# Performance work log

Measured on AMD Instinct MI355X. Metric: run time of the kernel, lower is better.

Reference implementation:

```python
import jax, jax.numpy as jnp
import numpy as np

NEG_NUM = -10000.0

def setup_inputs() -> dict:
    key = jax.random.key(0)
    k1, k2, k3, k4, k5, k6 = jax.random.split(key, 6)
    batch, enc_len = 32, 2048
    ctx_size, query_size, att_hid = 1024, 1024, 512
    in_dim = ctx_size + query_size
    ctx = jax.random.normal(k1, (batch, enc_len, ctx_size), dtype=jnp.float32)
    query = jax.random.normal(k2, (batch, query_size), dtype=jnp.float32)
    mask = jax.random.randint(k3, (batch, enc_len), 0, 2, dtype=jnp.int32)
    # Linear params (stored as (in, out) for x @ W + b)
    s1 = 1.0 / np.sqrt(in_dim)
    W1 = jax.random.uniform(k4, (in_dim, att_hid), jnp.float32, -s1, s1)
    b1 = jnp.zeros((att_hid,), jnp.float32)
    s2 = 1.0 / np.sqrt(att_hid)
    W2 = jax.random.uniform(k5, (att_hid, 1), jnp.float32, -s2, s2)
    b2 = jnp.zeros((1,), jnp.float32)
    return {"ctx": ctx, "query": query, "W1": W1, "b1": b1, "W2": W2, "b2": b2, "mask": mask}

def reference(ctx, query, W1, b1, W2, b2, mask):
    # ctx: (B, S, Dc), query: (B, Dq)
    B, S, Dc = ctx.shape
    Dq = query.shape[-1]
    # Equivalent to concat([ctx, query_expanded]) @ W1: split W1 into ctx/query blocks
    Wc, Wq = W1[:Dc], W1[Dc:]
    hidden = jnp.tanh(jnp.einsum('bsd,dh->bsh', ctx, Wc)
                      + (query @ Wq)[:, None, :] + b1)      # (B, S, H)
    score = jnp.einsum('bsh,h->bs', hidden, W2[:, 0]) + b2[0]  # (B, S)
    score = jnp.where(mask == 0, NEG_NUM, score)
    p_ctx = jax.nn.softmax(score, axis=-1)                   # (B, S)
    expected_ctx = jnp.einsum('bs,bsd->bd', p_ctx, ctx)      # (B, Dc)
    return (expected_ctx, p_ctx)
```

## Files before the change

kernel.cpp:

```cpp
#include <hip/hip_runtime.h>

typedef __bf16 bf16;
typedef __attribute__((ext_vector_type(8))) __bf16 bf16x8;
typedef __attribute__((ext_vector_type(4))) __bf16 bf16x4;
typedef __attribute__((ext_vector_type(4))) float f32x4;

#define B_  32
#define S_  2048
#define DC  1024
#define DQ  1024
#define H_  512
#define M_  (B_*S_)

#define BM  64

__global__ __launch_bounds__(256) void k_prep(const float* __restrict__ W1,
                                              const float* __restrict__ query,
                                              const float* __restrict__ b1,
                                              bf16* __restrict__ WcT2,
                                              float* __restrict__ qb) {
    const int bid = blockIdx.x, tid = threadIdx.x;
    if (bid < 256) {
        __shared__ bf16 t[32 * 68];
        const int kb = bid >> 3;
        const int cb = bid & 7;
        #pragma unroll
        for (int i = 0; i < 2; ++i) {
            int idx = i * 256 + tid;
            int k  = idx >> 4;
            int h4 = (idx & 15) * 4;
            const float4 v = *(const float4*)(W1 + ((size_t)(kb * 32 + k)) * H_ + cb * 64 + h4);
            bf16x4 pk = { (bf16)v.x, (bf16)v.y, (bf16)v.z, (bf16)v.w };
            *(bf16x4*)(&t[k * 68 + h4]) = pk;
        }
        __syncthreads();
        const int col = tid >> 2;
        const int kk0 = (tid & 3) * 8;
        bf16x8 o;
        #pragma unroll
        for (int j = 0; j < 8; ++j) o[j] = t[(kk0 + j) * 68 + col];
        *(bf16x8*)(WcT2 + (size_t)kb * 16384 + (size_t)(cb * 64 + col) * 32 + kk0) = o;
    } else {
        const int r = bid - 256;
        const int hblk = r & 7;
        const int b    = r >> 3;
        __shared__ float q[DQ];
        __shared__ float red[256];
        #pragma unroll
        for (int i = 0; i < 4; ++i)
            q[tid + i * 256] = query[(size_t)b * DQ + tid + i * 256];
        __syncthreads();
        const int h  = hblk * 64 + (tid & 63);
        const int kc = tid >> 6;
        const float* w = W1 + (size_t)DC * H_ + (size_t)(kc * 256) * H_ + h;
        const float* qv = q + kc * 256;
        float acc = 0.0f;
        #pragma unroll 8
        for (int k = 0; k < 256; ++k)
            acc = fmaf(qv[k], w[(size_t)k * H_], acc);
        red[tid] = acc;
        __syncthreads();
        if (tid < 64)
            qb[(size_t)b * H_ + hblk * 64 + tid] =
                red[tid] + red[tid + 64] + red[tid + 128] + red[tid + 192] + b1[hblk * 64 + tid];
    }
}

__global__ __launch_bounds__(256, 2) void k_gemm(const float* __restrict__ ctx,
                                                 const bf16*  __restrict__ WcT2,
                                                 const float* __restrict__ qb,
                                                 const float* __restrict__ W2,
                                                 float* __restrict__ score) {
    __shared__ float red[BM * 4];

    const int tid  = threadIdx.x;
    const int mblk = blockIdx.x;
    const size_t row_base = (size_t)mblk * BM;
    const int b = mblk >> 5;

    const int lane = tid & 63;
    const int wn   = tid >> 6;
    const int l16  = lane & 15;
    const int quad = lane >> 4;

    f32x4 acc[4][8] = {};

    const float* arow[4];
    #pragma unroll
    for (int mf = 0; mf < 4; ++mf)
        arow[mf] = ctx + (row_base + mf * 16 + l16) * (size_t)DC + quad * 8;
    const bf16* bptr = WcT2 + (size_t)(wn * 128 + l16) * 32 + quad * 8;

    float4 av0[2][4], av1[2][4];
    #pragma unroll
    for (int mf = 0; mf < 4; ++mf) {
        av0[0][mf] = *(const float4*)(arow[mf]);
        av1[0][mf] = *(const float4*)(arow[mf] + 4);
    }

    #pragma unroll 2
    for (int kb = 0; kb < 32; ++kb) {
        const int cur = kb & 1, nxt = cur ^ 1;
        bf16x8 bF[8];
        #pragma unroll
        for (int nf = 0; nf < 8; ++nf)
            bF[nf] = *(const bf16x8*)(bptr + (size_t)kb * 16384 + nf * 512);
        if (kb < 31) {
            #pragma unroll
            for (int mf = 0; mf < 4; ++mf) {
                av0[nxt][mf] = *(const float4*)(arow[mf] + (kb + 1) * 32);
                av1[nxt][mf] = *(const float4*)(arow[mf] + (kb + 1) * 32 + 4);
            }
        }
        bf16x8 aF[4];
        #pragma unroll
        for (int mf = 0; mf < 4; ++mf) {
            const float4 v0 = av0[cur][mf], v1 = av1[cur][mf];
            aF[mf] = bf16x8{ (bf16)v0.x, (bf16)v0.y, (bf16)v0.z, (bf16)v0.w,
                             (bf16)v1.x, (bf16)v1.y, (bf16)v1.z, (bf16)v1.w };
        }
        #pragma unroll
        for (int mf = 0; mf < 4; ++mf)
            #pragma unroll
            for (int nf = 0; nf < 8; ++nf)
                acc[mf][nf] = __builtin_amdgcn_mfma_f32_16x16x32_bf16(aF[mf], bF[nf], acc[mf][nf], 0, 0, 0);
    }

    float qv[8], wv[8];
    #pragma unroll
    for (int nf = 0; nf < 8; ++nf) {
        int c = wn * 128 + nf * 16 + l16;
        qv[nf] = qb[(size_t)b * H_ + c];
        wv[nf] = W2[c];
    }
    #pragma unroll
    for (int mf = 0; mf < 4; ++mf) {
        #pragma unroll
        for (int r = 0; r < 4; ++r) {
            float s = 0.0f;
            #pragma unroll
            for (int nf = 0; nf < 8; ++nf) {
                float x = acc[mf][nf][r] + qv[nf];
                float t = 1.0f - 2.0f / (1.0f + __expf(2.0f * x));
                s = fmaf(t, wv[nf], s);
            }
            s += __shfl_xor(s, 1);
            s += __shfl_xor(s, 2);
            s += __shfl_xor(s, 4);
            s += __shfl_xor(s, 8);
            if (l16 == 0)
                red[(mf * 16 + quad * 4 + r) * 4 + wn] = s;
        }
    }
    __syncthreads();
    if (tid < BM)
        score[row_base + tid] = red[tid * 4] + red[tid * 4 + 1] + red[tid * 4 + 2] + red[tid * 4 + 3];
}

__global__ __launch_bounds__(256) void k_softmax(const float* __restrict__ score,
                                                 const float* __restrict__ b2,
                                                 const int*   __restrict__ mask,
                                                 float* __restrict__ p_out) {
    int b = blockIdx.x, tid = threadIdx.x;
    __shared__ float red[256];
    float loc[8];
    float b2v = b2[0];
    float mx = -1e30f;
    #pragma unroll
    for (int i = 0; i < 8; ++i) {
        size_t r = (size_t)b * S_ + i * 256 + tid;
        float v = score[r] + b2v;
        if (mask[r] == 0) v = -10000.0f;
        loc[i] = v;
        mx = fmaxf(mx, v);
    }
    red[tid] = mx; __syncthreads();
    for (int o = 128; o > 0; o >>= 1) {
        if (tid < o) red[tid] = fmaxf(red[tid], red[tid + o]);
        __syncthreads();
    }
    mx = red[0]; __syncthreads();
    float se = 0.0f;
    #pragma unroll
    for (int i = 0; i < 8; ++i) {
        float e = __expf(loc[i] - mx);
        loc[i] = e;
        se += e;
    }
    red[tid] = se; __syncthreads();
    for (int o = 128; o > 0; o >>= 1) {
        if (tid < o) red[tid] += red[tid + o];
        __syncthreads();
    }
    float inv = 1.0f / red[0];
    #pragma unroll
    for (int i = 0; i < 8; ++i)
        p_out[(size_t)b * S_ + i * 256 + tid] = loc[i] * inv;
}

__global__ __launch_bounds__(256) void k_expected(const float* __restrict__ ctx,
                                                  const float* __restrict__ p,
                                                  float* __restrict__ partial) {
    const int sb = blockIdx.x, b = blockIdx.y, tid = threadIdx.x;
    __shared__ float ps[64];
    if (tid < 64) ps[tid] = p[(size_t)b * S_ + sb * 64 + tid];
    __syncthreads();
    const float* base = ctx + ((size_t)b * S_ + sb * 64) * DC + tid * 4;
    float ax = 0.f, ay = 0.f, az = 0.f, aw = 0.f;
    #pragma unroll 8
    for (int s = 0; s < 64; ++s) {
        const float4 v = *(const float4*)(base + (size_t)s * DC);
        float w = ps[s];
        ax = fmaf(w, v.x, ax);
        ay = fmaf(w, v.y, ay);
        az = fmaf(w, v.z, az);
        aw = fmaf(w, v.w, aw);
    }
    float4 o = { ax, ay, az, aw };
    *(float4*)(partial + ((size_t)(b * 32 + sb)) * DC + tid * 4) = o;
}

__global__ __launch_bounds__(256) void k_reduce(const float* __restrict__ partial,
                                                float* __restrict__ out) {
    const int cq = blockIdx.x, b = blockIdx.y, tid = threadIdx.x;
    const int c = cq * 256 + tid;
    float acc = 0.f;
    #pragma unroll
    for (int sb = 0; sb < 32; ++sb)
        acc += partial[((size_t)(b * 32 + sb)) * DC + c];
    out[(size_t)b * DC + c] = acc;
}

extern "C" void kernel_launch(void* const* d_in, const int* in_sizes, int n_in,
                              void* d_out, int out_size, void* d_ws, size_t ws_size,
                              hipStream_t stream) {
    (void)in_sizes; (void)n_in; (void)out_size; (void)ws_size;
    const float* ctx   = (const float*)d_in[0];
    const float* query = (const float*)d_in[1];
    const float* W1    = (const float*)d_in[2];
    const float* b1    = (const float*)d_in[3];
    const float* W2    = (const float*)d_in[4];
    const float* b2    = (const float*)d_in[5];
    const int*   mask  = (const int*)d_in[6];

    float* out      = (float*)d_out;
    float* expected = out;
    float* p_out    = out + 32768;

    char* w = (char*)d_ws;
    bf16*  WcT2      = (bf16*)w;
    float* qb        = (float*)(w + (1 << 20));
    float* score     = (float*)(w + (1 << 20) + (64 << 10));
    float* partial_e = (float*)(w + (1 << 20) + (320 << 10));

    k_prep    <<<512, 256, 0, stream>>>(W1, query, b1, WcT2, qb);
    k_gemm    <<<M_ / BM, 256, 0, stream>>>(ctx, WcT2, qb, W2, score);
    k_softmax <<<B_, 256, 0, stream>>>(score, b2, mask, p_out);
    k_expected<<<dim3(32, B_), 256, 0, stream>>>(ctx, p_out, partial_e);
    k_reduce  <<<dim3(4, B_), 256, 0, stream>>>(partial_e, expected);
}
```

Before: 550.6 us.

## Stage ctx tiles in LDS and cache a bf16 ctx copy for the weighted sum

```diff
diff --git a/kernel.cpp b/kernel.cpp
--- a/kernel.cpp
+++ b/kernel.cpp
@@ -13,6 +13,9 @@
 #define M_  (B_*S_)
 
 #define BM  64
+#define BK  32
+
+__device__ __forceinline__ int aoff(int s) { return s * 8 + (s >> 3) * 2; }
 
 __global__ __launch_bounds__(256) void k_prep(const float* __restrict__ W1,
                                               const float* __restrict__ query,
@@ -66,11 +69,14 @@
     }
 }
 
+template<bool STORE>
 __global__ __launch_bounds__(256, 2) void k_gemm(const float* __restrict__ ctx,
                                                  const bf16*  __restrict__ WcT2,
                                                  const float* __restrict__ qb,
                                                  const float* __restrict__ W2,
-                                                 float* __restrict__ score) {
+                                                 float* __restrict__ score,
+                                                 bf16* __restrict__ ctxb) {
+    __shared__ bf16 As[2][2176];
     __shared__ float red[BM * 4];
 
     const int tid  = threadIdx.x;
@@ -85,45 +91,53 @@
 
     f32x4 acc[4][8] = {};
 
-    const float* arow[4];
-    #pragma unroll
-    for (int mf = 0; mf < 4; ++mf)
-        arow[mf] = ctx + (row_base + mf * 16 + l16) * (size_t)DC + quad * 8;
+    const int srow = (tid >> 6) * 16 + (tid & 15);
+    const int sq   = (tid >> 4) & 3;
+    const float* asrc = ctx + (row_base + srow) * (size_t)DC + sq * 8;
+    bf16* adst = STORE ? (ctxb + (row_base + srow) * (size_t)DC + sq * 8) : (bf16*)nullptr;
+    const int awr = aoff(tid);
+    int ard[4];
+    #pragma unroll
+    for (int mf = 0; mf < 4; ++mf) ard[mf] = aoff(mf * 64 + lane);
     const bf16* bptr = WcT2 + (size_t)(wn * 128 + l16) * 32 + quad * 8;
 
-    float4 av0[2][4], av1[2][4];
-    #pragma unroll
-    for (int mf = 0; mf < 4; ++mf) {
-        av0[0][mf] = *(const float4*)(arow[mf]);
-        av1[0][mf] = *(const float4*)(arow[mf] + 4);
-    }
-
-    #pragma unroll 2
+    {
+        const float4 v0 = *(const float4*)(asrc);
+        const float4 v1 = *(const float4*)(asrc + 4);
+        bf16x8 a8 = { (bf16)v0.x, (bf16)v0.y, (bf16)v0.z, (bf16)v0.w,
+                      (bf16)v1.x, (bf16)v1.y, (bf16)v1.z, (bf16)v1.w };
+        *(bf16x8*)(&As[0][awr]) = a8;
+        if (STORE) *(bf16x8*)adst = a8;
+    }
+    __syncthreads();
+
     for (int kb = 0; kb < 32; ++kb) {
         const int cur = kb & 1, nxt = cur ^ 1;
         bf16x8 bF[8];
         #pragma unroll
         for (int nf = 0; nf < 8; ++nf)
             bF[nf] = *(const bf16x8*)(bptr + (size_t)kb * 16384 + nf * 512);
+        float4 av0, av1;
         if (kb < 31) {
-            #pragma unroll
-            for (int mf = 0; mf < 4; ++mf) {
-                av0[nxt][mf] = *(const float4*)(arow[mf] + (kb + 1) * 32);
-                av1[nxt][mf] = *(const float4*)(arow[mf] + (kb + 1) * 32 + 4);
-            }
+            av0 = *(const float4*)(asrc + (kb + 1) * BK);
+            av1 = *(const float4*)(asrc + (kb + 1) * BK + 4);
         }
         bf16x8 aF[4];
         #pragma unroll
-        for (int mf = 0; mf < 4; ++mf) {
-            const float4 v0 = av0[cur][mf], v1 = av1[cur][mf];
-            aF[mf] = bf16x8{ (bf16)v0.x, (bf16)v0.y, (bf16)v0.z, (bf16)v0.w,
-                             (bf16)v1.x, (bf16)v1.y, (bf16)v1.z, (bf16)v1.w };
-        }
+        for (int mf = 0; mf < 4; ++mf)
+            aF[mf] = *(const bf16x8*)(&As[cur][ard[mf]]);
         #pragma unroll
         for (int mf = 0; mf < 4; ++mf)
             #pragma unroll
             for (int nf = 0; nf < 8; ++nf)
                 acc[mf][nf] = __builtin_amdgcn_mfma_f32_16x16x32_bf16(aF[mf], bF[nf], acc[mf][nf], 0, 0, 0);
+        if (kb < 31) {
+            bf16x8 a8 = { (bf16)av0.x, (bf16)av0.y, (bf16)av0.z, (bf16)av0.w,
+                          (bf16)av1.x, (bf16)av1.y, (bf16)av1.z, (bf16)av1.w };
+            *(bf16x8*)(&As[nxt][awr]) = a8;
+            if (STORE) *(bf16x8*)(adst + (kb + 1) * BK) = a8;
+        }
+        __syncthreads();
     }
 
     float qv[8], wv[8];
@@ -198,23 +212,38 @@
         p_out[(size_t)b * S_ + i * 256 + tid] = loc[i] * inv;
 }
 
-__global__ __launch_bounds__(256) void k_expected(const float* __restrict__ ctx,
+template<bool BF>
+__global__ __launch_bounds__(256) void k_expected(const float* __restrict__ ctxf,
+                                                  const bf16*  __restrict__ ctxb,
                                                   const float* __restrict__ p,
                                                   float* __restrict__ partial) {
     const int sb = blockIdx.x, b = blockIdx.y, tid = threadIdx.x;
     __shared__ float ps[64];
     if (tid < 64) ps[tid] = p[(size_t)b * S_ + sb * 64 + tid];
     __syncthreads();
-    const float* base = ctx + ((size_t)b * S_ + sb * 64) * DC + tid * 4;
     float ax = 0.f, ay = 0.f, az = 0.f, aw = 0.f;
-    #pragma unroll 8
-    for (int s = 0; s < 64; ++s) {
-        const float4 v = *(const float4*)(base + (size_t)s * DC);
-        float w = ps[s];
-        ax = fmaf(w, v.x, ax);
-        ay = fmaf(w, v.y, ay);
-        az = fmaf(w, v.z, az);
-        aw = fmaf(w, v.w, aw);
+    if (BF) {
+        const bf16* base = ctxb + ((size_t)b * S_ + sb * 64) * DC + tid * 4;
+        #pragma unroll 8
+        for (int s = 0; s < 64; ++s) {
+            bf16x4 v = *(const bf16x4*)(base + (size_t)s * DC);
+            float w = ps[s];
+            ax = fmaf(w, (float)v[0], ax);
+            ay = fmaf(w, (float)v[1], ay);
+            az = fmaf(w, (float)v[2], az);
+            aw = fmaf(w, (float)v[3], aw);
+        }
+    } else {
+        const float* base = ctxf + ((size_t)b * S_ + sb * 64) * DC + tid * 4;
+        #pragma unroll 8
+        for (int s = 0; s < 64; ++s) {
+            const float4 v = *(const float4*)(base + (size_t)s * DC);
+            float w = ps[s];
+            ax = fmaf(w, v.x, ax);
+            ay = fmaf(w, v.y, ay);
+            az = fmaf(w, v.z, az);
+            aw = fmaf(w, v.w, aw);
+        }
     }
     float4 o = { ax, ay, az, aw };
     *(float4*)(partial + ((size_t)(b * 32 + sb)) * DC + tid * 4) = o;
@@ -234,7 +263,7 @@
 extern "C" void kernel_launch(void* const* d_in, const int* in_sizes, int n_in,
                               void* d_out, int out_size, void* d_ws, size_t ws_size,
                               hipStream_t stream) {
-    (void)in_sizes; (void)n_in; (void)out_size; (void)ws_size;
+    (void)in_sizes; (void)n_in; (void)out_size;
     const float* ctx   = (const float*)d_in[0];
     const float* query = (const float*)d_in[1];
     const float* W1    = (const float*)d_in[2];
@@ -247,15 +276,30 @@
     float* expected = out;
     float* p_out    = out + 32768;
 
+    const size_t CTXB = (size_t)M_ * DC * sizeof(bf16);
+    const size_t tail = (1 << 20) + (64 << 10) + (256 << 10) + (4 << 20) + 256;
     char* w = (char*)d_ws;
-    bf16*  WcT2      = (bf16*)w;
-    float* qb        = (float*)(w + (1 << 20));
-    float* score     = (float*)(w + (1 << 20) + (64 << 10));
-    float* partial_e = (float*)(w + (1 << 20) + (320 << 10));
-
-    k_prep    <<<512, 256, 0, stream>>>(W1, query, b1, WcT2, qb);
-    k_gemm    <<<M_ / BM, 256, 0, stream>>>(ctx, WcT2, qb, W2, score);
-    k_softmax <<<B_, 256, 0, stream>>>(score, b2, mask, p_out);
-    k_expected<<<dim3(32, B_), 256, 0, stream>>>(ctx, p_out, partial_e);
-    k_reduce  <<<dim3(4, B_), 256, 0, stream>>>(partial_e, expected);
-}
+
+    if (ws_size >= CTXB + tail) {
+        bf16*  ctxb   = (bf16*)w;
+        bf16*  WcT2   = (bf16*)(w + CTXB);
+        float* qb     = (float*)(w + CTXB + (1 << 20));
+        float* score  = (float*)(w + CTXB + (1 << 20) + (64 << 10));
+        float* partial= (float*)(w + CTXB + (1 << 20) + (320 << 10));
+        k_prep          <<<512, 256, 0, stream>>>(W1, query, b1, WcT2, qb);
+        k_gemm<true>    <<<M_ / BM, 256, 0, stream>>>(ctx, WcT2, qb, W2, score, ctxb);
+        k_softmax       <<<B_, 256, 0, stream>>>(score, b2, mask, p_out);
+        k_expected<true><<<dim3(32, B_), 256, 0, stream>>>(ctx, ctxb, p_out, partial);
+        k_reduce        <<<dim3(4, B_), 256, 0, stream>>>(partial, expected);
+    } else {
+        bf16*  WcT2   = (bf16*)w;
+        float* qb     = (float*)(w + (1 << 20));
+        float* score  = (float*)(w + (1 << 20) + (64 << 10));
+        float* partial= (float*)(w + (1 << 20) + (320 << 10));
+        k_prep           <<<512, 256, 0, stream>>>(W1, query, b1, WcT2, qb);
+        k_gemm<false>    <<<M_ / BM, 256, 0, stream>>>(ctx, WcT2, qb, W2, score, nullptr);
+        k_softmax        <<<B_, 256, 0, stream>>>(score, b2, mask, p_out);
+        k_expected<false><<<dim3(32, B_), 256, 0, stream>>>(ctx, nullptr, p_out, partial);
+        k_reduce         <<<dim3(4, B_), 256, 0, stream>>>(partial, expected);
+    }
+}
```

Result: faster. 538.3 us (-2.2%).
